# Performance work log

Hardware: AMD Instinct MI355X
Metric: run time of the kernel (lower is better)

The kernel has to match this reference:

```python
import jax, jax.numpy as jnp
import numpy as np

N, Q, D = 16384, 16384, 3
RADIUS = 0.08  # ~30 expected neighbors for uniform points in [0,1]^3


def setup_inputs() -> dict:
    key = jax.random.key(0)
    k1, k2 = jax.random.split(key)
    data = jax.random.uniform(k1, (N, D), dtype=jnp.float32)
    queries = jax.random.uniform(k2, (Q, D), dtype=jnp.float32)
    return {"data": data, "queries": queries, "radius": RADIUS}


def reference(data, queries, radius):
    # Pairwise squared Euclidean distances [Q, N] via ||q||^2 + ||d||^2 - 2 q.d
    # (avoids materializing the [Q, N, D] difference tensor).
    q2 = jnp.sum(queries * queries, axis=-1)[:, None]   # [Q, 1]
    d2 = jnp.sum(data * data, axis=-1)[None, :]         # [1, N]
    sqdist = jnp.maximum(q2 + d2 - 2.0 * (queries @ data.T), 0.0)  # [Q, N]

    # Ball query: dist <= radius  <=>  sqdist <= radius^2 (sklearn query_radius semantics)
    mask = sqdist <= (radius * radius)                  # [Q, N] bool

    # Ragged row splits: [0, cumsum(per-query neighbor counts)] -> [Q+1]
    counts = jnp.sum(mask.astype(jnp.int32), axis=1)    # [Q]
    row_splits = jnp.concatenate(
        [jnp.zeros((1,), dtype=jnp.int32), jnp.cumsum(counts)]
    )

    # weights = squared distance for in-radius pairs (dense padded form of the
    # torch module's concatenated ragged 'weights' = dist**2)
    weights = jnp.where(mask, sqdist, jnp.float32(0.0))  # [Q, N]

    return mask, row_splits, weights
```

## Files before the change

kernel.cpp:

```cpp
#include <hip/hip_runtime.h>
#include <cstddef>


namespace {

constexpr int NPTS = 16384;
constexpr int NQ   = 16384;
constexpr int QB   = 8;
constexpr int TPB  = 256;
constexpr int VEC  = 8;
constexpr int ITERS = NPTS / (TPB * VEC);

__device__ __forceinline__ float norm2(float x, float y, float z) {
    return __fmaf_rn(x, x, __fmaf_rn(y, y, __fmul_rn(z, z)));
}

__device__ __forceinline__ float sqdist(float qx, float qy, float qz, float q2,
                                        float dx, float dy, float dz, float d2) {
    const float dot = __fmaf_rn(qx, dx, __fmaf_rn(qy, dy, __fmul_rn(qz, dz)));
    const float s   = __fmaf_rn(-2.0f, dot, __fadd_rn(q2, d2));
    return fmaxf(s, 0.0f);
}

__global__ __launch_bounds__(TPB) void ball_kernel(
    const float* __restrict__ data,
    const float* __restrict__ queries,
    const float* __restrict__ radius_p,
    float* __restrict__ out,
    int* __restrict__ counts)
{
    const int tid  = threadIdx.x;
    const int lane = tid & 63;
    const int q0   = blockIdx.x * QB;

    __shared__ float qs[(QB + 1) * 3];
    __shared__ int   scnt[QB];
    if (tid < (QB + 1) * 3) {
        int src = q0 * 3 - 3 + tid;
        if (src < 0) src = 0;
        qs[tid] = queries[src];
    }
    if (tid < QB) scnt[tid] = 0;
    __syncthreads();

    const float r  = radius_p[0];
    const float r2 = __fmul_rn(r, r);

    const float lxx = data[(size_t)(NPTS - 1) * 3 + 0];
    const float lyy = data[(size_t)(NPTS - 1) * 3 + 1];
    const float lzz = data[(size_t)(NPTS - 1) * 3 + 2];
    const float l2  = norm2(lxx, lyy, lzz);

    float* __restrict__ mask = out;
    float* __restrict__ wts  = out + ((size_t)NQ * NPTS + NQ + 1);

#pragma unroll 1
    for (int q = 0; q < QB; ++q) {
        const float qxq = qs[3 * (q + 1) + 0];
        const float qyq = qs[3 * (q + 1) + 1];
        const float qzq = qs[3 * (q + 1) + 2];
        const float q2q = norm2(qxq, qyq, qzq);

        const float px = qs[3 * q + 0], py = qs[3 * q + 1], pz = qs[3 * q + 2];
        const float sqh = sqdist(px, py, pz, norm2(px, py, pz), lxx, lyy, lzz, l2);
        const float wheadq = (sqh <= r2) ? sqh : 0.0f;

        float* __restrict__ mrow = mask + (size_t)(q0 + q) * NPTS;
        float* __restrict__ wrow = wts  + (size_t)(q0 + q) * NPTS;

        int cnt = 0;

#pragma unroll 1
        for (int it = 0; it < ITERS; ++it) {
            const int nb = (it * TPB + tid) * VEC;
            const float* dbase = data + (size_t)nb * 3;
            const float4 dA = *reinterpret_cast<const float4*>(dbase + 0);
            const float4 dB = *reinterpret_cast<const float4*>(dbase + 4);
            const float4 dC = *reinterpret_cast<const float4*>(dbase + 8);
            const float4 dD = *reinterpret_cast<const float4*>(dbase + 12);
            const float4 dE = *reinterpret_cast<const float4*>(dbase + 16);
            const float4 dF = *reinterpret_cast<const float4*>(dbase + 20);

            const int pm1 = (nb == 0) ? 0 : nb - 1;
            const float mx = data[(size_t)pm1 * 3 + 0];
            const float my = data[(size_t)pm1 * 3 + 1];
            const float mz = data[(size_t)pm1 * 3 + 2];

            const float dx[VEC] = {dA.x, dA.w, dB.z, dC.y, dD.x, dD.w, dE.z, dF.y};
            const float dy[VEC] = {dA.y, dB.x, dB.w, dC.z, dD.y, dE.x, dE.w, dF.z};
            const float dz[VEC] = {dA.z, dB.y, dC.x, dC.w, dD.z, dE.y, dF.x, dF.w};

            float m[VEC], w[VEC];
#pragma unroll
            for (int j = 0; j < VEC; ++j) {
                const float d2 = norm2(dx[j], dy[j], dz[j]);
                const float sq = sqdist(qxq, qyq, qzq, q2q, dx[j], dy[j], dz[j], d2);
                const bool in = (sq <= r2);
                m[j] = in ? 1.0f : 0.0f;
                w[j] = in ? sq : 0.0f;
                cnt += in ? 1 : 0;
            }

            const float m2  = norm2(mx, my, mz);
            const float sqm = sqdist(qxq, qyq, qzq, q2q, mx, my, mz, m2);
            const float wprev = (sqm <= r2) ? sqm : 0.0f;
            const float wsh = __shfl_up(w[7], 1);
            float slot0 = (lane == 0) ? wprev : wsh;
            if (tid == 0 && it == 0) slot0 = wheadq;

            *reinterpret_cast<float4*>(mrow + nb) =
                make_float4(m[0], m[1], m[2], m[3]);
            *reinterpret_cast<float4*>(mrow + nb + 4) =
                make_float4(m[4], m[5], m[6], m[7]);
            *reinterpret_cast<float4*>(wrow + nb - 1) =
                make_float4(slot0, w[0], w[1], w[2]);
            *reinterpret_cast<float4*>(wrow + nb + 3) =
                make_float4(w[3], w[4], w[5], w[6]);
        }

        for (int off = 32; off >= 1; off >>= 1) cnt += __shfl_down(cnt, off);
        if (lane == 0) atomicAdd(&scnt[q], cnt);
    }

    if (q0 == NQ - QB && tid == TPB - 1) {
        const float qxq = qs[3 * QB + 0];
        const float qyq = qs[3 * QB + 1];
        const float qzq = qs[3 * QB + 2];
        const float sq = sqdist(qxq, qyq, qzq, norm2(qxq, qyq, qzq),
                                lxx, lyy, lzz, l2);
        wts[(size_t)(NQ - 1) * NPTS + (NPTS - 1)] = (sq <= r2) ? sq : 0.0f;
    }

    __syncthreads();
    if (tid < QB) counts[q0 + tid] = scnt[tid];
}

constexpr int STPB  = 256;
constexpr int CHUNK = NQ / STPB;

__global__ __launch_bounds__(STPB) void scan_kernel(
    const int* __restrict__ counts, float* __restrict__ out)
{
    __shared__ int sums[STPB];
    const int tid  = threadIdx.x;
    const int base = tid * CHUNK;

    int s = 0;
    for (int i = 0; i < CHUNK; ++i) s += counts[base + i];
    sums[tid] = s;
    __syncthreads();

    for (int off = 1; off < STPB; off <<= 1) {
        int v = 0;
        if (tid >= off) v = sums[tid - off];
        __syncthreads();
        sums[tid] += v;
        __syncthreads();
    }

    int run = (tid == 0) ? 0 : sums[tid - 1];
    float* rs = out + (size_t)NQ * NPTS;
    if (tid == 0) rs[0] = 0.0f;
    for (int i = 0; i < CHUNK; ++i) {
        run += counts[base + i];
        rs[base + i + 1] = (float)run;
    }
}

}

extern "C" void kernel_launch(void* const* d_in, const int* in_sizes, int n_in,
                              void* d_out, int out_size, void* d_ws, size_t ws_size,
                              hipStream_t stream) {
    const float* data    = (const float*)d_in[0];
    const float* queries = (const float*)d_in[1];
    const float* radius  = (const float*)d_in[2];
    float* out  = (float*)d_out;
    int* counts = (int*)d_ws;

    hipLaunchKernelGGL(ball_kernel, dim3(NQ / QB), dim3(TPB), 0, stream,
                       data, queries, radius, out, counts);
    hipLaunchKernelGGL(scan_kernel, dim3(1), dim3(STPB), 0, stream, counts, out);
}
```

Baseline: 409.6 us.

## Split mask and weight writing into separate block sets, doubling grid

New measurement: 993.7 us. 2.43x slower.

```diff
diff --git a/kernel.cpp b/kernel.cpp
--- a/kernel.cpp
+++ b/kernel.cpp
@@ -10,6 +10,7 @@
 constexpr int TPB  = 256;
 constexpr int VEC  = 8;
 constexpr int ITERS = NPTS / (TPB * VEC);
+constexpr int NBLK  = NQ / QB;
 
 __device__ __forceinline__ float norm2(float x, float y, float z) {
     return __fmaf_rn(x, x, __fmaf_rn(y, y, __fmul_rn(z, z)));
@@ -31,7 +32,8 @@
 {
     const int tid  = threadIdx.x;
     const int lane = tid & 63;
-    const int q0   = blockIdx.x * QB;
+    const bool is_mask_blk = (blockIdx.x < NBLK);
+    const int q0   = (is_mask_blk ? blockIdx.x : blockIdx.x - NBLK) * QB;
 
     __shared__ float qs[(QB + 1) * 3];
     __shared__ int   scnt[QB];
@@ -46,93 +48,128 @@
     const float r  = radius_p[0];
     const float r2 = __fmul_rn(r, r);
 
-    const float lxx = data[(size_t)(NPTS - 1) * 3 + 0];
-    const float lyy = data[(size_t)(NPTS - 1) * 3 + 1];
-    const float lzz = data[(size_t)(NPTS - 1) * 3 + 2];
-    const float l2  = norm2(lxx, lyy, lzz);
-
     float* __restrict__ mask = out;
     float* __restrict__ wts  = out + ((size_t)NQ * NPTS + NQ + 1);
 
-#pragma unroll 1
-    for (int q = 0; q < QB; ++q) {
-        const float qxq = qs[3 * (q + 1) + 0];
-        const float qyq = qs[3 * (q + 1) + 1];
-        const float qzq = qs[3 * (q + 1) + 2];
-        const float q2q = norm2(qxq, qyq, qzq);
-
-        const float px = qs[3 * q + 0], py = qs[3 * q + 1], pz = qs[3 * q + 2];
-        const float sqh = sqdist(px, py, pz, norm2(px, py, pz), lxx, lyy, lzz, l2);
-        const float wheadq = (sqh <= r2) ? sqh : 0.0f;
-
-        float* __restrict__ mrow = mask + (size_t)(q0 + q) * NPTS;
-        float* __restrict__ wrow = wts  + (size_t)(q0 + q) * NPTS;
-
-        int cnt = 0;
-
-#pragma unroll 1
-        for (int it = 0; it < ITERS; ++it) {
-            const int nb = (it * TPB + tid) * VEC;
-            const float* dbase = data + (size_t)nb * 3;
-            const float4 dA = *reinterpret_cast<const float4*>(dbase + 0);
-            const float4 dB = *reinterpret_cast<const float4*>(dbase + 4);
-            const float4 dC = *reinterpret_cast<const float4*>(dbase + 8);
-            const float4 dD = *reinterpret_cast<const float4*>(dbase + 12);
-            const float4 dE = *reinterpret_cast<const float4*>(dbase + 16);
-            const float4 dF = *reinterpret_cast<const float4*>(dbase + 20);
-
-            const int pm1 = (nb == 0) ? 0 : nb - 1;
-            const float mx = data[(size_t)pm1 * 3 + 0];
-            const float my = data[(size_t)pm1 * 3 + 1];
-            const float mz = data[(size_t)pm1 * 3 + 2];
-
-            const float dx[VEC] = {dA.x, dA.w, dB.z, dC.y, dD.x, dD.w, dE.z, dF.y};
-            const float dy[VEC] = {dA.y, dB.x, dB.w, dC.z, dD.y, dE.x, dE.w, dF.z};
-            const float dz[VEC] = {dA.z, dB.y, dC.x, dC.w, dD.z, dE.y, dF.x, dF.w};
-
-            float m[VEC], w[VEC];
+    if (is_mask_blk) {
+#pragma unroll 1
+        for (int q = 0; q < QB; ++q) {
+            const float qxq = qs[3 * (q + 1) + 0];
+            const float qyq = qs[3 * (q + 1) + 1];
+            const float qzq = qs[3 * (q + 1) + 2];
+            const float q2q = norm2(qxq, qyq, qzq);
+
+            float* __restrict__ mrow = mask + (size_t)(q0 + q) * NPTS;
+            int cnt = 0;
+
+#pragma unroll 1
+            for (int it = 0; it < ITERS; ++it) {
+                const int nb = (it * TPB + tid) * VEC;
+                const float* dbase = data + (size_t)nb * 3;
+                const float4 dA = *reinterpret_cast<const float4*>(dbase + 0);
+                const float4 dB = *reinterpret_cast<const float4*>(dbase + 4);
+                const float4 dC = *reinterpret_cast<const float4*>(dbase + 8);
+                const float4 dD = *reinterpret_cast<const float4*>(dbase + 12);
+                const float4 dE = *reinterpret_cast<const float4*>(dbase + 16);
+                const float4 dF = *reinterpret_cast<const float4*>(dbase + 20);
+                const float dx[VEC] = {dA.x, dA.w, dB.z, dC.y, dD.x, dD.w, dE.z, dF.y};
+                const float dy[VEC] = {dA.y, dB.x, dB.w, dC.z, dD.y, dE.x, dE.w, dF.z};
+                const float dz[VEC] = {dA.z, dB.y, dC.x, dC.w, dD.z, dE.y, dF.x, dF.w};
+
+                float m[VEC];
 #pragma unroll
-            for (int j = 0; j < VEC; ++j) {
-                const float d2 = norm2(dx[j], dy[j], dz[j]);
-                const float sq = sqdist(qxq, qyq, qzq, q2q, dx[j], dy[j], dz[j], d2);
-                const bool in = (sq <= r2);
-                m[j] = in ? 1.0f : 0.0f;
-                w[j] = in ? sq : 0.0f;
-                cnt += in ? 1 : 0;
+                for (int j = 0; j < VEC; ++j) {
+                    const float d2 = norm2(dx[j], dy[j], dz[j]);
+                    const float sq = sqdist(qxq, qyq, qzq, q2q,
+                                            dx[j], dy[j], dz[j], d2);
+                    const bool in = (sq <= r2);
+                    m[j] = in ? 1.0f : 0.0f;
+                    cnt += in ? 1 : 0;
+                }
+                *reinterpret_cast<float4*>(mrow + nb) =
+                    make_float4(m[0], m[1], m[2], m[3]);
+                *reinterpret_cast<float4*>(mrow + nb + 4) =
+                    make_float4(m[4], m[5], m[6], m[7]);
             }
 
-            const float m2  = norm2(mx, my, mz);
-            const float sqm = sqdist(qxq, qyq, qzq, q2q, mx, my, mz, m2);
-            const float wprev = (sqm <= r2) ? sqm : 0.0f;
-            const float wsh = __shfl_up(w[7], 1);
-            float slot0 = (lane == 0) ? wprev : wsh;
-            if (tid == 0 && it == 0) slot0 = wheadq;
-
-            *reinterpret_cast<float4*>(mrow + nb) =
-                make_float4(m[0], m[1], m[2], m[3]);
-            *reinterpret_cast<float4*>(mrow + nb + 4) =
-                make_float4(m[4], m[5], m[6], m[7]);
-            *reinterpret_cast<float4*>(wrow + nb - 1) =
-                make_float4(slot0, w[0], w[1], w[2]);
-            *reinterpret_cast<float4*>(wrow + nb + 3) =
-                make_float4(w[3], w[4], w[5], w[6]);
+            for (int off = 32; off >= 1; off >>= 1) cnt += __shfl_down(cnt, off);
+            if (lane == 0) atomicAdd(&scnt[q], cnt);
         }
-
-        for (int off = 32; off >= 1; off >>= 1) cnt += __shfl_down(cnt, off);
-        if (lane == 0) atomicAdd(&scnt[q], cnt);
-    }
-
-    if (q0 == NQ - QB && tid == TPB - 1) {
-        const float qxq = qs[3 * QB + 0];
-        const float qyq = qs[3 * QB + 1];
-        const float qzq = qs[3 * QB + 2];
-        const float sq = sqdist(qxq, qyq, qzq, norm2(qxq, qyq, qzq),
-                                lxx, lyy, lzz, l2);
-        wts[(size_t)(NQ - 1) * NPTS + (NPTS - 1)] = (sq <= r2) ? sq : 0.0f;
-    }
-
-    __syncthreads();
-    if (tid < QB) counts[q0 + tid] = scnt[tid];
+        __syncthreads();
+        if (tid < QB) counts[q0 + tid] = scnt[tid];
+
+    } else {
+        const float lxx = data[(size_t)(NPTS - 1) * 3 + 0];
+        const float lyy = data[(size_t)(NPTS - 1) * 3 + 1];
+        const float lzz = data[(size_t)(NPTS - 1) * 3 + 2];
+        const float l2  = norm2(lxx, lyy, lzz);
+
+#pragma unroll 1
+        for (int q = 0; q < QB; ++q) {
+            const float qxq = qs[3 * (q + 1) + 0];
+            const float qyq = qs[3 * (q + 1) + 1];
+            const float qzq = qs[3 * (q + 1) + 2];
+            const float q2q = norm2(qxq, qyq, qzq);
+
+            const float px = qs[3 * q + 0], py = qs[3 * q + 1], pz = qs[3 * q + 2];
+            const float sqh = sqdist(px, py, pz, norm2(px, py, pz),
+                                     lxx, lyy, lzz, l2);
+            const float wheadq = (sqh <= r2) ? sqh : 0.0f;
+
+            float* __restrict__ wrow = wts + (size_t)(q0 + q) * NPTS;
+
+#pragma unroll 1
+            for (int it = 0; it < ITERS; ++it) {
+                const int nb = (it * TPB + tid) * VEC;
+                const float* dbase = data + (size_t)nb * 3;
+                const float4 dA = *reinterpret_cast<const float4*>(dbase + 0);
+                const float4 dB = *reinterpret_cast<const float4*>(dbase + 4);
+                const float4 dC = *reinterpret_cast<const float4*>(dbase + 8);
+                const float4 dD = *reinterpret_cast<const float4*>(dbase + 12);
+                const float4 dE = *reinterpret_cast<const float4*>(dbase + 16);
+                const float4 dF = *reinterpret_cast<const float4*>(dbase + 20);
+
+                const int pm1 = (nb == 0) ? 0 : nb - 1;
+                const float mx = data[(size_t)pm1 * 3 + 0];
+                const float my = data[(size_t)pm1 * 3 + 1];
+                const float mz = data[(size_t)pm1 * 3 + 2];
+
+                const float dx[VEC] = {dA.x, dA.w, dB.z, dC.y, dD.x, dD.w, dE.z, dF.y};
+                const float dy[VEC] = {dA.y, dB.x, dB.w, dC.z, dD.y, dE.x, dE.w, dF.z};
+                const float dz[VEC] = {dA.z, dB.y, dC.x, dC.w, dD.z, dE.y, dF.x, dF.w};
+
+                float w[VEC];
+#pragma unroll
+                for (int j = 0; j < VEC; ++j) {
+                    const float d2 = norm2(dx[j], dy[j], dz[j]);
+                    const float sq = sqdist(qxq, qyq, qzq, q2q,
+                                            dx[j], dy[j], dz[j], d2);
+                    w[j] = (sq <= r2) ? sq : 0.0f;
+                }
+
+                const float m2  = norm2(mx, my, mz);
+                const float sqm = sqdist(qxq, qyq, qzq, q2q, mx, my, mz, m2);
+                const float wprev = (sqm <= r2) ? sqm : 0.0f;
+                const float wsh = __shfl_up(w[7], 1);
+                float slot0 = (lane == 0) ? wprev : wsh;
+                if (tid == 0 && it == 0) slot0 = wheadq;
+
+                *reinterpret_cast<float4*>(wrow + nb - 1) =
+                    make_float4(slot0, w[0], w[1], w[2]);
+                *reinterpret_cast<float4*>(wrow + nb + 3) =
+                    make_float4(w[3], w[4], w[5], w[6]);
+            }
+        }
+
+        if (q0 == NQ - QB && tid == TPB - 1) {
+            const float qxq = qs[3 * QB + 0];
+            const float qyq = qs[3 * QB + 1];
+            const float qzq = qs[3 * QB + 2];
+            const float sq = sqdist(qxq, qyq, qzq, norm2(qxq, qyq, qzq),
+                                    lxx, lyy, lzz, l2);
+            wts[(size_t)(NQ - 1) * NPTS + (NPTS - 1)] = (sq <= r2) ? sq : 0.0f;
+        }
+    }
 }
 
 constexpr int STPB  = 256;
@@ -178,7 +215,7 @@
     float* out  = (float*)d_out;
     int* counts = (int*)d_ws;
 
-    hipLaunchKernelGGL(ball_kernel, dim3(NQ / QB), dim3(TPB), 0, stream,
+    hipLaunchKernelGGL(ball_kernel, dim3(2 * NBLK), dim3(TPB), 0, stream,
                        data, queries, radius, out, counts);
     hipLaunchKernelGGL(scan_kernel, dim3(1), dim3(STPB), 0, stream, counts, out);
 }
```
